# Performance work log

Measured on AMD Instinct MI355X. Metric: run time of the kernel, lower is better.

Reference implementation:

```python
import jax, jax.numpy as jnp
import numpy as np

T, B, I, H, E, C = 256, 64, 1024, 1024, 4, 128
STDV = 1.0 / np.sqrt(H)


def setup_inputs() -> dict:
    key = jax.random.key(0)
    ks = jax.random.split(key, 8)
    x_seq = jax.random.normal(ks[0], (T, B, I), dtype=jnp.float32)
    h0 = jnp.zeros((1, B, H), dtype=jnp.float32)
    c0 = jnp.zeros((1, B, H), dtype=jnp.float32)
    coef = jax.random.uniform(ks[1], (B, E), dtype=jnp.float32)
    # expert params (uniform(-stdv, stdv) init as in the torch module)
    u = lambda k, shp: jax.random.uniform(k, shp, dtype=jnp.float32, minval=-STDV, maxval=STDV)
    Wi = u(ks[2], (E, 4 * H, I))
    bi = u(ks[3], (E, 4 * H))
    Wh = u(ks[4], (E, 4 * H, H))
    bh = u(ks[5], (E, 4 * H))
    Wo = u(ks[6], (E, C, H))
    bo = u(ks[7], (E, C))
    return {"x_seq": x_seq, "h0": h0, "c0": c0, "coef": coef,
            "Wi": Wi, "bi": bi, "Wh": Wh, "bh": bh, "Wo": Wo, "bo": bo}


def reference(x_seq, h0, c0, coef, Wi, bi, Wh, bh, Wo, bo):
    # MoO with IDGate == per-sample convex combination of expert linear outputs,
    # which equals a linear layer with per-sample mixed weights.
    # Precompute mixed input projections for all timesteps: [T,B,4H]
    xi = jnp.einsum('tbi,eoi,be->tbo', x_seq, Wi, coef) + coef @ bi
    # Per-sample mixed hidden weights: [B,4H,H] and bias [B,4H]
    Whm = jnp.einsum('eoi,be->boi', Wh, coef)
    bhm = coef @ bh

    def step(carry, xg):
        h, c = carry
        gates = xg + jnp.einsum('bi,boi->bo', h, Whm) + bhm  # [B,4H]
        ig, fg, gg, og = jnp.split(gates, 4, axis=-1)  # i,f,g,o order as in torch chunk
        c = jax.nn.sigmoid(fg) * c + jax.nn.sigmoid(ig) * jnp.tanh(gg)
        h = jax.nn.sigmoid(og) * jnp.tanh(c)
        return (h, c), h

    (hT, cT), hs = jax.lax.scan(step, (h0[0], c0[0]), xi)  # hs: [T,B,H]
    # h2o: mixed output projection (activation is identity, dropout p=0)
    out = jnp.einsum('tbh,ech,be->tbc', hs, Wo, coef) + coef @ bo  # [T,B,C]
    return out, hT[None], cT[None]
```

## Files before the change

kernel.cpp:

```cpp
#include <hip/hip_runtime.h>
#include <hip/hip_fp16.h>
#include <cstdint>

#define T_  256
#define B_  64
#define I_  1024
#define H_  1024
#define E_  4
#define C_  128
#define G4  4096

typedef _Float16 f16;
typedef _Float16 f16x2 __attribute__((ext_vector_type(2)));
typedef _Float16 f16x8 __attribute__((ext_vector_type(8)));
typedef float    f32x4 __attribute__((ext_vector_type(4)));

__device__ __forceinline__ float sigmoidf_(float x) { return 1.f / (1.f + __expf(-x)); }

union pk2 { uint32_t u; f16x2 h; };

__global__ void k_f32_to_f16(const float* __restrict__ src, f16* __restrict__ dst, int n8) {
    int i = blockIdx.x * blockDim.x + threadIdx.x;
    int stride = gridDim.x * blockDim.x;
    for (; i < n8; i += stride) {
        const float4* s = reinterpret_cast<const float4*>(src) + (size_t)i * 2;
        float4 a = s[0], b = s[1];
        f16x8 v = { (f16)a.x, (f16)a.y, (f16)a.z, (f16)a.w,
                    (f16)b.x, (f16)b.y, (f16)b.z, (f16)b.w };
        *reinterpret_cast<f16x8*>(dst + (size_t)i * 8) = v;
    }
}

__global__ void k_mix_biases(const float* __restrict__ coef, const float* __restrict__ bi,
                             const float* __restrict__ bh, const float* __restrict__ bo,
                             float* __restrict__ gbias, float* __restrict__ bom) {
    int idx = blockIdx.x * blockDim.x + threadIdx.x;
    int stride = gridDim.x * blockDim.x;
    for (int i = idx; i < B_ * G4; i += stride) {
        int b = i >> 12, o = i & (G4 - 1);
        float s = 0.f;
#pragma unroll
        for (int e = 0; e < 4; ++e) s += coef[b * 4 + e] * (bi[e * G4 + o] + bh[e * G4 + o]);
        gbias[i] = s;
    }
    for (int i = idx; i < B_ * C_; i += stride) {
        int b = i >> 7, c = i & (C_ - 1);
        float s = 0.f;
#pragma unroll
        for (int e = 0; e < 4; ++e) s += coef[b * 4 + e] * bo[e * C_ + c];
        bom[i] = s;
    }
}

__global__ void k_init_h0h(const float* __restrict__ h0, f16* __restrict__ h0h) {
    int i = blockIdx.x * blockDim.x + threadIdx.x;
    if (i < B_ * H_) h0h[i] = (f16)h0[i];
}

template<bool XF16, bool WF16>
__global__ __launch_bounds__(256, 1) void k_xi_gemm(
        const f16* __restrict__ xh, const float* __restrict__ xf,
        const f16* __restrict__ Wih, const float* __restrict__ Wif,
        const float* __restrict__ coef, const float* __restrict__ gbias,
        f16* __restrict__ xi) {
    __shared__ f16 As[256 * 72];
    __shared__ f16 Bs[128 * 72];
    const int nt = blockIdx.x;
    const int b  = blockIdx.y;
    const int tid = threadIdx.x;
    const int lane = tid & 63, wave = tid >> 6;
    const int wr = wave >> 1, wc = wave & 1;

    float cf[4];
#pragma unroll
    for (int e = 0; e < 4; ++e) cf[e] = coef[b * 4 + e];

    f32x4 acc[8][4];
#pragma unroll
    for (int mi = 0; mi < 8; ++mi)
#pragma unroll
        for (int ni = 0; ni < 4; ++ni) acc[mi][ni] = 0.f;

    for (int kk = 0; kk < I_; kk += 64) {
        __syncthreads();
#pragma unroll
        for (int it = 0; it < 8; ++it) {
            int chunk = it * 256 + tid;
            int row = chunk >> 3, c8 = chunk & 7;
            if constexpr (XF16) {
                *reinterpret_cast<f16x8*>(&As[row * 72 + c8 * 8]) =
                    *reinterpret_cast<const f16x8*>(&xh[((size_t)row * B_ + b) * I_ + kk + c8 * 8]);
            } else {
                const float4* p = reinterpret_cast<const float4*>(&xf[((size_t)row * B_ + b) * I_ + kk + c8 * 8]);
                float4 a = p[0], bq = p[1];
                f16x8 v = { (f16)a.x, (f16)a.y, (f16)a.z, (f16)a.w,
                            (f16)bq.x, (f16)bq.y, (f16)bq.z, (f16)bq.w };
                *reinterpret_cast<f16x8*>(&As[row * 72 + c8 * 8]) = v;
            }
        }
#pragma unroll
        for (int it = 0; it < 4; ++it) {
            int chunk = it * 256 + tid;
            int n = chunk >> 3, c8 = chunk & 7;
            if constexpr (WF16) {
                size_t base = ((size_t)(nt * 128 + n)) * I_ + kk + c8 * 8;
                f16 c0 = (f16)cf[0], c1 = (f16)cf[1], c2 = (f16)cf[2], c3 = (f16)cf[3];
                f16x8 w0 = *reinterpret_cast<const f16x8*>(&Wih[base]);
                f16x8 w1 = *reinterpret_cast<const f16x8*>(&Wih[base + (size_t)1 * G4 * I_]);
                f16x8 w2 = *reinterpret_cast<const f16x8*>(&Wih[base + (size_t)2 * G4 * I_]);
                f16x8 w3 = *reinterpret_cast<const f16x8*>(&Wih[base + (size_t)3 * G4 * I_]);
                f16x8 m = w0 * c0 + w1 * c1 + w2 * c2 + w3 * c3;
                *reinterpret_cast<f16x8*>(&Bs[n * 72 + c8 * 8]) = m;
            } else {
                size_t base = ((size_t)(nt * 128 + n)) * I_ + kk + c8 * 8;
                float m[8];
#pragma unroll
                for (int j = 0; j < 8; ++j) m[j] = 0.f;
#pragma unroll
                for (int e = 0; e < 4; ++e) {
                    const float4* p = reinterpret_cast<const float4*>(&Wif[base + (size_t)e * G4 * I_]);
                    float4 a = p[0], bq = p[1];
                    m[0] += cf[e] * a.x;  m[1] += cf[e] * a.y;
                    m[2] += cf[e] * a.z;  m[3] += cf[e] * a.w;
                    m[4] += cf[e] * bq.x; m[5] += cf[e] * bq.y;
                    m[6] += cf[e] * bq.z; m[7] += cf[e] * bq.w;
                }
                f16x8 v = { (f16)m[0], (f16)m[1], (f16)m[2], (f16)m[3],
                            (f16)m[4], (f16)m[5], (f16)m[6], (f16)m[7] };
                *reinterpret_cast<f16x8*>(&Bs[n * 72 + c8 * 8]) = v;
            }
        }
        __syncthreads();
#pragma unroll
        for (int ks = 0; ks < 2; ++ks) {
            int ko = ks * 32 + (lane >> 4) * 8;
            f16x8 a[8], bb[4];
#pragma unroll
            for (int mi = 0; mi < 8; ++mi)
                a[mi] = *reinterpret_cast<const f16x8*>(&As[(wr * 128 + mi * 16 + (lane & 15)) * 72 + ko]);
#pragma unroll
            for (int ni = 0; ni < 4; ++ni)
                bb[ni] = *reinterpret_cast<const f16x8*>(&Bs[(wc * 64 + ni * 16 + (lane & 15)) * 72 + ko]);
#pragma unroll
            for (int mi = 0; mi < 8; ++mi)
#pragma unroll
                for (int ni = 0; ni < 4; ++ni)
                    acc[mi][ni] = __builtin_amdgcn_mfma_f32_16x16x32_f16(a[mi], bb[ni], acc[mi][ni], 0, 0, 0);
        }
    }
#pragma unroll
    for (int mi = 0; mi < 8; ++mi)
#pragma unroll
        for (int ni = 0; ni < 4; ++ni)
#pragma unroll
            for (int j = 0; j < 4; ++j) {
                int t = wr * 128 + mi * 16 + (lane >> 4) * 4 + j;
                int o = nt * 128 + wc * 64 + ni * 16 + (lane & 15);
                float v = acc[mi][ni][j] + gbias[b * G4 + o];
                xi[((size_t)t * B_ + b) * G4 + o] = (f16)v;
            }
}

#define POOL_SZ  163840
#define A0_OFF   131072
#define A1_OFF   (131072 + 8192)
#define A2_OFF   (131072 + 16384)
#define A3_OFF   (131072 + 24576)
#define GL_OFF   131072

#define BF(KC, KS) (*reinterpret_cast<const f16x8*>(pool + wrow + (KC) * 128 + (((KS) * 64 + koff) ^ swz)))
#define PRE(KC, PF) PF = *reinterpret_cast<const f16x8*>(&hprev[(size_t)sr * hstr + (KC) * 64 + soct * 8]);
#define AFR(AOFF, AROW, KS) (*reinterpret_cast<const f16x8*>(pool + (AOFF) + (AROW) + (((KS) * 64 + koff) ^ swz)))
#define WRA(AOFF, PF) *reinterpret_cast<f16x8*>(pool + (AOFF) + sdst) = PF;

#define MM4(ROFF, BQ0, BQ1) \
    acc0 = __builtin_amdgcn_mfma_f32_16x16x32_f16(AFR(ROFF, arow0, 0), BQ0, acc0, 0, 0, 0); \
    acc1 = __builtin_amdgcn_mfma_f32_16x16x32_f16(AFR(ROFF, arow1, 0), BQ0, acc1, 0, 0, 0); \
    acc0 = __builtin_amdgcn_mfma_f32_16x16x32_f16(AFR(ROFF, arow0, 1), BQ1, acc0, 0, 0, 0); \
    acc1 = __builtin_amdgcn_mfma_f32_16x16x32_f16(AFR(ROFF, arow1, 1), BQ1, acc1, 0, 0, 0);

#define TPW(KC, RB, PK, PL, PW, WB) { \
    const f16x8 bq0 = BF(KC, 0), bq1 = BF(KC, 1); \
    PRE(PK, PL); \
    MM4(RB, bq0, bq1); \
    WRA(WB, PW); \
}
#define TW(KC, RB, PW, WB) { \
    const f16x8 bq0 = BF(KC, 0), bq1 = BF(KC, 1); \
    MM4(RB, bq0, bq1); \
    WRA(WB, PW); \
}
#define TN(KC, RB) { \
    const f16x8 bq0 = BF(KC, 0), bq1 = BF(KC, 1); \
    MM4(RB, bq0, bq1); \
}

#define GO2IDX(T, KC, L) ((((size_t)(T) * 16 + (KC)) * 16 + (L)) * 16)

__device__ __forceinline__ void pollgo(const int* p) {
    while (__hip_atomic_load(p, __ATOMIC_RELAXED, __HIP_MEMORY_SCOPE_AGENT) == 0)
        __builtin_amdgcn_s_sleep(1);
}

__global__ __launch_bounds__(512, 1) void k_rec_persist(
        const float* __restrict__ Wh, const f16* __restrict__ h0h,
        const float* __restrict__ c0, f16* xi, const float* __restrict__ coef,
        float* __restrict__ out, int* __restrict__ arr, int* __restrict__ go2) {
    __shared__ __attribute__((aligned(16))) char pool[POOL_SZ];
    float* gl = reinterpret_cast<float*>(pool + GL_OFF);

    const int bid = blockIdx.x;
    const int jb = ((bid & 7) << 5) | (bid >> 3);
    const int tid = threadIdx.x, lane = tid & 63, w = tid >> 6;
    const int ex = w & 3, mh = w >> 2;
    const int l15 = lane & 15, hi8 = (lane >> 4) * 8;
    const int myTile = jb >> 4;
    const int goLine = bid & 15;

    for (int i = tid; i < 8192; i += 512) {
        int r = i >> 7, oct = i & 127;
        int e = r >> 4, g = (r >> 2) & 3, c = r & 3;
        const float* src = &Wh[((size_t)e * G4 + g * H_ + jb * 4 + c) * H_ + oct * 8];
        float4 f0 = *reinterpret_cast<const float4*>(src);
        float4 f1 = *reinterpret_cast<const float4*>(src + 4);
        f16x8 v = { (f16)f0.x, (f16)f0.y, (f16)f0.z, (f16)f0.w,
                    (f16)f1.x, (f16)f1.y, (f16)f1.z, (f16)f1.w };
        int db = r * 2048 + ((oct * 16) ^ ((r & 7) << 4));
        *reinterpret_cast<f16x8*>(pool + db) = v;
    }

    const int bb = tid >> 1, pr = tid & 1;
    const int cp0 = jb * 4 + pr * 2;
    float c_reg0 = 0.f, c_reg1 = 0.f;
    float4 cf4 = {0.f, 0.f, 0.f, 0.f};
    if (tid < 128) {
        c_reg0 = c0[bb * H_ + cp0];
        c_reg1 = c0[bb * H_ + cp0 + 1];
        cf4 = *reinterpret_cast<const float4*>(&coef[bb * 4]);
    }

    const int swz   = (l15 & 7) << 4;
    const int koff  = hi8 * 2;
    const int wrow  = (ex * 16 + l15) * 2048;
    const int arow0 = (mh * 32 + l15) * 128;
    const int arow1 = arow0 + 16 * 128;
    const int sr = tid >> 3, soct = tid & 7;
    const int sdst = sr * 128 + ((soct * 16) ^ ((sr & 7) << 4));

    __syncthreads();

    float xgc0a = 0.f, xgc0b = 0.f, xgc1a = 0.f, xgc1b = 0.f;
    float xgc2a = 0.f, xgc2b = 0.f, xgc3a = 0.f, xgc3b = 0.f;
    if (tid < 128) {
        const f16* xp = &xi[((size_t)0 * B_ + bb) * G4 + cp0];
        pk2 p0; p0.u = __hip_atomic_load(reinterpret_cast<const uint32_t*>(xp),
                                         __ATOMIC_RELAXED, __HIP_MEMORY_SCOPE_AGENT);
        xgc0a = (float)p0.h.x; xgc0b = (float)p0.h.y;
        f16x2 g1 = *reinterpret_cast<const f16x2*>(xp + H_);
        f16x2 g2 = *reinterpret_cast<const f16x2*>(xp + 2 * H_);
        f16x2 g3 = *reinterpret_cast<const f16x2*>(xp + 3 * H_);
        xgc1a = (float)g1.x; xgc1b = (float)g1.y;
        xgc2a = (float)g2.x; xgc2b = (float)g2.y;
        xgc3a = (float)g3.x; xgc3b = (float)g3.y;
    }

    for (int t = 0; t < T_; ++t) {
        const f16* hprev = (t == 0) ? h0h : (xi + (size_t)(t - 1) * B_ * G4);
        const size_t hstr = (t == 0) ? (size_t)H_ : (size_t)G4;

        if (t > 0) {
            if (tid < 8) pollgo(&go2[GO2IDX(t - 1, tid, goLine)]);
            __builtin_amdgcn_sched_barrier(0);
            __syncthreads();
        }

        f16x8 pfa, pfb, pfc, pfd;
        PRE(0, pfa) PRE(1, pfb) PRE(2, pfc) PRE(3, pfd)

        float xgn0a = 0.f, xgn0b = 0.f, xgn1a = 0.f, xgn1b = 0.f;
        float xgn2a = 0.f, xgn2b = 0.f, xgn3a = 0.f, xgn3b = 0.f;
        if (t + 1 < T_ && tid < 128) {
            const f16* xq = &xi[((size_t)(t + 1) * B_ + bb) * G4 + cp0];
            pk2 p0; p0.u = __hip_atomic_load(reinterpret_cast<const uint32_t*>(xq),
                                             __ATOMIC_RELAXED, __HIP_MEMORY_SCOPE_AGENT);
            xgn0a = (float)p0.h.x; xgn0b = (float)p0.h.y;
            f16x2 g1 = *reinterpret_cast<const f16x2*>(xq + H_);
            f16x2 g2 = *reinterpret_cast<const f16x2*>(xq + 2 * H_);
            f16x2 g3 = *reinterpret_cast<const f16x2*>(xq + 3 * H_);
            xgn1a = (float)g1.x; xgn1b = (float)g1.y;
            xgn2a = (float)g2.x; xgn2b = (float)g2.y;
            xgn3a = (float)g3.x; xgn3b = (float)g3.y;
        }

        WRA(A0_OFF, pfa)
        WRA(A1_OFF, pfb)
        f32x4 acc0 = {0.f, 0.f, 0.f, 0.f}, acc1 = {0.f, 0.f, 0.f, 0.f};
        __syncthreads();

        if (t > 0 && tid < 4) pollgo(&go2[GO2IDX(t - 1, 8 + tid, goLine)]);
        TPW(0, A0_OFF, 4, pfa, pfc, A2_OFF)
        TPW(1, A1_OFF, 5, pfb, pfd, A3_OFF)
        __syncthreads();
        TPW(2, A2_OFF, 6, pfc, pfa, A0_OFF)
        TPW(3, A3_OFF, 7, pfd, pfb, A1_OFF)
        __syncthreads();
        if (t > 0 && tid < 4) pollgo(&go2[GO2IDX(t - 1, 12 + tid, goLine)]);
        TPW(4, A0_OFF, 8, pfa, pfc, A2_OFF)
        TPW(5, A1_OFF, 9, pfb, pfd, A3_OFF)
        __syncthreads();
        TPW(6, A2_OFF, 10, pfc, pfa, A0_OFF)
        TPW(7, A3_OFF, 11, pfd, pfb, A1_OFF)
        __syncthreads();
        TPW(8, A0_OFF, 12, pfa, pfc, A2_OFF)
        TPW(9, A1_OFF, 13, pfb, pfd, A3_OFF)
        __syncthreads();
        TPW(10, A2_OFF, 14, pfc, pfa, A0_OFF)
        TPW(11, A3_OFF, 15, pfd, pfb, A1_OFF)
        __syncthreads();
        TW(12, A0_OFF, pfc, A2_OFF)
        TW(13, A1_OFF, pfd, A3_OFF)
        __syncthreads();
        TN(14, A2_OFF)
        TN(15, A3_OFF)
        __syncthreads();

#pragma unroll
        for (int j = 0; j < 4; ++j) {
            int r0 = mh * 32 + (lane >> 4) * 4 + j;
            gl[(ex * 64 + r0) * 17 + l15]      = acc0[j];
            gl[(ex * 64 + r0 + 16) * 17 + l15] = acc1[j];
        }
        __syncthreads();

        if (tid < 128) {
            float ga[4], gb[4];
#pragma unroll
            for (int g = 0; g < 4; ++g) {
                int nn = g * 4 + pr * 2;
                ga[g] = cf4.x * gl[(0 * 64 + bb) * 17 + nn] +
                        cf4.y * gl[(1 * 64 + bb) * 17 + nn] +
                        cf4.z * gl[(2 * 64 + bb) * 17 + nn] +
                        cf4.w * gl[(3 * 64 + bb) * 17 + nn];
                gb[g] = cf4.x * gl[(0 * 64 + bb) * 17 + nn + 1] +
                        cf4.y * gl[(1 * 64 + bb) * 17 + nn + 1] +
                        cf4.z * gl[(2 * 64 + bb) * 17 + nn + 1] +
                        cf4.w * gl[(3 * 64 + bb) * 17 + nn + 1];
            }
            ga[0] += xgc0a; ga[1] += xgc1a; ga[2] += xgc2a; ga[3] += xgc3a;
            gb[0] += xgc0b; gb[1] += xgc1b; gb[2] += xgc2b; gb[3] += xgc3b;
            float cn0 = sigmoidf_(ga[1]) * c_reg0 + sigmoidf_(ga[0]) * tanhf(ga[2]);
            float hn0 = sigmoidf_(ga[3]) * tanhf(cn0);
            float cn1 = sigmoidf_(gb[1]) * c_reg1 + sigmoidf_(gb[0]) * tanhf(gb[2]);
            float hn1 = sigmoidf_(gb[3]) * tanhf(cn1);
            c_reg0 = cn0; c_reg1 = cn1;
            pk2 st; st.h.x = (f16)hn0; st.h.y = (f16)hn1;
            __hip_atomic_store(reinterpret_cast<uint32_t*>(&xi[((size_t)t * B_ + bb) * G4 + cp0]),
                               st.u, __ATOMIC_RELAXED, __HIP_MEMORY_SCOPE_AGENT);
            if (t == T_ - 1) {
                out[(size_t)T_ * B_ * C_ + bb * H_ + cp0]     = hn0;
                out[(size_t)T_ * B_ * C_ + bb * H_ + cp0 + 1] = hn1;
                out[(size_t)T_ * B_ * C_ + B_ * H_ + bb * H_ + cp0]     = cn0;
                out[(size_t)T_ * B_ * C_ + B_ * H_ + bb * H_ + cp0 + 1] = cn1;
            }
        }
        xgc0a = xgn0a; xgc0b = xgn0b; xgc1a = xgn1a; xgc1b = xgn1b;
        xgc2a = xgn2a; xgc2b = xgn2b; xgc3a = xgn3a; xgc3b = xgn3b;

        if (t < T_ - 1) {
            __syncthreads();
            if (tid == 0)
                __hip_atomic_store(&arr[t * 256 + jb], 1, __ATOMIC_RELAXED,
                                   __HIP_MEMORY_SCOPE_AGENT);
            __syncthreads();
            if (tid < 64) {
                int v = 1;
                if (lane < 16)
                    v = __hip_atomic_load(&arr[t * 256 + myTile * 16 + lane],
                                          __ATOMIC_RELAXED, __HIP_MEMORY_SCOPE_AGENT);
                unsigned long long m = __ballot(v != 0);
                if (m == ~0ull && lane < 16)
                    __hip_atomic_store(&go2[GO2IDX(t, myTile, lane)], 1,
                                       __ATOMIC_RELAXED, __HIP_MEMORY_SCOPE_AGENT);
            }
        }
    }
}

__global__ __launch_bounds__(256, 1) void k_out_gemm(
        const f16* __restrict__ hs, const f16* __restrict__ Woh,
        const float* __restrict__ coef, const float* __restrict__ bom,
        float* __restrict__ out) {
    __shared__ f16 As[64 * 72];
    __shared__ f16 Bs[256 * 72];
    __shared__ float cfs[64][4];
    const int nt = blockIdx.x;
    const int t  = blockIdx.y;
    const int tid = threadIdx.x, lane = tid & 63, w = tid >> 6;
    cfs[tid >> 2][tid & 3] = coef[tid];

    f32x4 acc[4][4];
#pragma unroll
    for (int e = 0; e < 4; ++e)
#pragma unroll
        for (int mi = 0; mi < 4; ++mi) acc[e][mi] = 0.f;

    for (int kk = 0; kk < H_; kk += 64) {
        __syncthreads();
#pragma unroll
        for (int it = 0; it < 2; ++it) {
            int chunk = it * 256 + tid;
            int row = chunk >> 3, c8 = chunk & 7;
            *reinterpret_cast<f16x8*>(&As[row * 72 + c8 * 8]) =
                *reinterpret_cast<const f16x8*>(&hs[((size_t)t * B_ + row) * G4 + kk + c8 * 8]);
        }
#pragma unroll
        for (int it = 0; it < 8; ++it) {
            int chunk = it * 256 + tid;
            int r = chunk >> 3, c8 = chunk & 7;
            int e = r >> 6, nn = r & 63;
            size_t grow = (size_t)e * C_ + nt * 64 + nn;
            *reinterpret_cast<f16x8*>(&Bs[r * 72 + c8 * 8]) =
                *reinterpret_cast<const f16x8*>(&Woh[grow * H_ + kk + c8 * 8]);
        }
        __syncthreads();
#pragma unroll
        for (int ks = 0; ks < 2; ++ks) {
            int ko = ks * 32 + (lane >> 4) * 8;
            f16x8 a[4];
#pragma unroll
            for (int mi = 0; mi < 4; ++mi)
                a[mi] = *reinterpret_cast<const f16x8*>(&As[(mi * 16 + (lane & 15)) * 72 + ko]);
#pragma unroll
            for (int e = 0; e < 4; ++e) {
                f16x8 bf = *reinterpret_cast<const f16x8*>(&Bs[(e * 64 + w * 16 + (lane & 15)) * 72 + ko]);
#pragma unroll
                for (int mi = 0; mi < 4; ++mi)
                    acc[e][mi] = __builtin_amdgcn_mfma_f32_16x16x32_f16(a[mi], bf, acc[e][mi], 0, 0, 0);
            }
        }
    }
#pragma unroll
    for (int mi = 0; mi < 4; ++mi)
#pragma unroll
        for (int j = 0; j < 4; ++j) {
            int bb = mi * 16 + (lane >> 4) * 4 + j;
            int cc = nt * 64 + w * 16 + (lane & 15);
            float v = cfs[bb][0] * acc[0][mi][j] + cfs[bb][1] * acc[1][mi][j] +
                      cfs[bb][2] * acc[2][mi][j] + cfs[bb][3] * acc[3][mi][j];
            v += bom[bb * C_ + cc];
            out[((size_t)t * B_ + bb) * C_ + cc] = v;
        }
}

extern "C" void kernel_launch(void* const* d_in, const int* in_sizes, int n_in,
                              void* d_out, int out_size, void* d_ws, size_t ws_size,
                              hipStream_t stream) {
    const float* x    = (const float*)d_in[0];
    const float* h0   = (const float*)d_in[1];
    const float* c0   = (const float*)d_in[2];
    const float* coef = (const float*)d_in[3];
    const float* Wi   = (const float*)d_in[4];
    const float* bi   = (const float*)d_in[5];
    const float* Wh   = (const float*)d_in[6];
    const float* bh   = (const float*)d_in[7];
    const float* Wo   = (const float*)d_in[8];
    const float* bo   = (const float*)d_in[9];
    float* out = (float*)d_out;

    char* base = (char*)d_ws;
    size_t off = 0;
    auto carve = [&](size_t bytes) -> char* {
        char* r = base + off;
        off = (off + bytes + 255) & ~(size_t)255;
        return r;
    };
    const size_t SZ_XI  = (size_t)T_ * B_ * G4 * 2;
    const size_t SZ_WOH = (size_t)E_ * C_ * H_ * 2;
    const size_t SZ_ARR = (size_t)T_ * 256 * 4;
    const size_t SZ_GO2 = (size_t)T_ * 16 * 16 * 16 * 4;
    const size_t SZ_WIH = (size_t)E_ * G4 * I_ * 2;
    const size_t SZ_XH  = (size_t)T_ * B_ * I_ * 2;

    f16*   xi     = (f16*)carve(SZ_XI);
    f16*   Woh    = (f16*)carve(SZ_WOH);
    f16*   h0h    = (f16*)carve((size_t)B_ * H_ * 2);
    float* gbias  = (float*)carve((size_t)B_ * G4 * 4);
    float* bom    = (float*)carve((size_t)B_ * C_ * 4);
    int*   arr    = (int*)carve(SZ_ARR);
    int*   go2    = (int*)carve(SZ_GO2);

    f16* Wih = nullptr;
    f16* xh  = nullptr;
    if (off + SZ_WIH + 256 <= ws_size) Wih = (f16*)carve(SZ_WIH);
    if (Wih && off + SZ_XH + 256 <= ws_size) xh = (f16*)carve(SZ_XH);
    (void)in_sizes; (void)n_in; (void)out_size;

    hipMemsetAsync(arr, 0, SZ_ARR, stream);
    hipMemsetAsync(go2, 0, SZ_GO2, stream);

    if (xh)  k_f32_to_f16<<<2048, 256, 0, stream>>>(x,  xh,  (T_ * B_ * I_) / 8);
    if (Wih) k_f32_to_f16<<<2048, 256, 0, stream>>>(Wi, Wih, (E_ * G4 * I_) / 8);
    k_f32_to_f16<<<512,  256, 0, stream>>>(Wo, Woh, (E_ * C_ * H_) / 8);
    k_mix_biases<<<512, 256, 0, stream>>>(coef, bi, bh, bo, gbias, bom);
    k_init_h0h<<<(B_ * H_ + 255) / 256, 256, 0, stream>>>(h0, h0h);

    dim3 gx(32, 64);
    if (xh)
        k_xi_gemm<true,  true ><<<gx, 256, 0, stream>>>(xh, nullptr, Wih, nullptr, coef, gbias, xi);
    else if (Wih)
        k_xi_gemm<false, true ><<<gx, 256, 0, stream>>>(nullptr, x, Wih, nullptr, coef, gbias, xi);
    else
        k_xi_gemm<false, false><<<gx, 256, 0, stream>>>(nullptr, x, nullptr, Wi, coef, gbias, xi);

    {
        void* args[] = { (void*)&Wh, (void*)&h0h, (void*)&c0, (void*)&xi,
                         (void*)&coef, (void*)&out, (void*)&arr, (void*)&go2 };
        hipLaunchCooperativeKernel((const void*)k_rec_persist, dim3(256), dim3(512),
                                   args, 0, stream);
    }

    dim3 go_(2, 256);
    k_out_gemm<<<go_, 256, 0, stream>>>(xi, Woh, coef, bom, out);
}
```

Baseline: 2.261 ms.

## Replace two-level arrive/go flags with atomic fetch-or bitmask per tile

Each block now sets its bit with an atomic fetch_or on all 16 replicated go lines for its tile, and consumers poll all 16 tile words up front until each reads 0xFFFF. This replaces the arrive array, the leader aggregation via ballot and the staggered partial polls that overlapped the wait with the first MFMA chunks. The extra sync hop through a per-tile leader goes away, but every block now waits for all tiles before any compute, so there is no longer any overlap of the wait with early k-chunks. Contended atomics on shared words are also added.

```diff
diff --git a/kernel.cpp b/kernel.cpp
--- a/kernel.cpp
+++ b/kernel.cpp
@@ -195,17 +195,12 @@
     MM4(RB, bq0, bq1); \
 }
 
-#define GO2IDX(T, KC, L) ((((size_t)(T) * 16 + (KC)) * 16 + (L)) * 16)
-
-__device__ __forceinline__ void pollgo(const int* p) {
-    while (__hip_atomic_load(p, __ATOMIC_RELAXED, __HIP_MEMORY_SCOPE_AGENT) == 0)
-        __builtin_amdgcn_s_sleep(1);
-}
+#define GO3IDX(T, TILE, L) ((((size_t)(T) * 16 + (TILE)) * 16 + (L)) * 16)
 
 __global__ __launch_bounds__(512, 1) void k_rec_persist(
         const float* __restrict__ Wh, const f16* __restrict__ h0h,
         const float* __restrict__ c0, f16* xi, const float* __restrict__ coef,
-        float* __restrict__ out, int* __restrict__ arr, int* __restrict__ go2) {
+        float* __restrict__ out, int* __restrict__ go3) {
     __shared__ __attribute__((aligned(16))) char pool[POOL_SZ];
     float* gl = reinterpret_cast<float*>(pool + GL_OFF);
 
@@ -216,6 +211,7 @@
     const int l15 = lane & 15, hi8 = (lane >> 4) * 8;
     const int myTile = jb >> 4;
     const int goLine = bid & 15;
+    const int myBit  = 1 << (jb & 15);
 
     for (int i = tid; i < 8192; i += 512) {
         int r = i >> 7, oct = i & 127;
@@ -269,7 +265,12 @@
         const size_t hstr = (t == 0) ? (size_t)H_ : (size_t)G4;
 
         if (t > 0) {
-            if (tid < 8) pollgo(&go2[GO2IDX(t - 1, tid, goLine)]);
+            if (tid < 16) {
+                const int* p = &go3[GO3IDX(t - 1, tid, goLine)];
+                while (__hip_atomic_load(p, __ATOMIC_RELAXED, __HIP_MEMORY_SCOPE_AGENT)
+                       != 0xFFFF)
+                    __builtin_amdgcn_s_sleep(1);
+            }
             __builtin_amdgcn_sched_barrier(0);
             __syncthreads();
         }
@@ -297,14 +298,12 @@
         f32x4 acc0 = {0.f, 0.f, 0.f, 0.f}, acc1 = {0.f, 0.f, 0.f, 0.f};
         __syncthreads();
 
-        if (t > 0 && tid < 4) pollgo(&go2[GO2IDX(t - 1, 8 + tid, goLine)]);
         TPW(0, A0_OFF, 4, pfa, pfc, A2_OFF)
         TPW(1, A1_OFF, 5, pfb, pfd, A3_OFF)
         __syncthreads();
         TPW(2, A2_OFF, 6, pfc, pfa, A0_OFF)
         TPW(3, A3_OFF, 7, pfd, pfb, A1_OFF)
         __syncthreads();
-        if (t > 0 && tid < 4) pollgo(&go2[GO2IDX(t - 1, 12 + tid, goLine)]);
         TPW(4, A0_OFF, 8, pfa, pfc, A2_OFF)
         TPW(5, A1_OFF, 9, pfb, pfd, A3_OFF)
         __syncthreads();
@@ -368,20 +367,9 @@
 
         if (t < T_ - 1) {
             __syncthreads();
-            if (tid == 0)
-                __hip_atomic_store(&arr[t * 256 + jb], 1, __ATOMIC_RELAXED,
-                                   __HIP_MEMORY_SCOPE_AGENT);
-            __syncthreads();
-            if (tid < 64) {
-                int v = 1;
-                if (lane < 16)
-                    v = __hip_atomic_load(&arr[t * 256 + myTile * 16 + lane],
-                                          __ATOMIC_RELAXED, __HIP_MEMORY_SCOPE_AGENT);
-                unsigned long long m = __ballot(v != 0);
-                if (m == ~0ull && lane < 16)
-                    __hip_atomic_store(&go2[GO2IDX(t, myTile, lane)], 1,
-                                       __ATOMIC_RELAXED, __HIP_MEMORY_SCOPE_AGENT);
-            }
+            if (tid < 16)
+                __hip_atomic_fetch_or(&go3[GO3IDX(t, myTile, tid)], myBit,
+                                      __ATOMIC_RELEASE, __HIP_MEMORY_SCOPE_AGENT);
         }
     }
 }
@@ -476,8 +464,7 @@
     };
     const size_t SZ_XI  = (size_t)T_ * B_ * G4 * 2;
     const size_t SZ_WOH = (size_t)E_ * C_ * H_ * 2;
-    const size_t SZ_ARR = (size_t)T_ * 256 * 4;
-    const size_t SZ_GO2 = (size_t)T_ * 16 * 16 * 16 * 4;
+    const size_t SZ_GO3 = (size_t)T_ * 16 * 16 * 16 * 4;
     const size_t SZ_WIH = (size_t)E_ * G4 * I_ * 2;
     const size_t SZ_XH  = (size_t)T_ * B_ * I_ * 2;
 
@@ -486,8 +473,7 @@
     f16*   h0h    = (f16*)carve((size_t)B_ * H_ * 2);
     float* gbias  = (float*)carve((size_t)B_ * G4 * 4);
     float* bom    = (float*)carve((size_t)B_ * C_ * 4);
-    int*   arr    = (int*)carve(SZ_ARR);
-    int*   go2    = (int*)carve(SZ_GO2);
+    int*   go3    = (int*)carve(SZ_GO3);
 
     f16* Wih = nullptr;
     f16* xh  = nullptr;
@@ -495,8 +481,7 @@
     if (Wih && off + SZ_XH + 256 <= ws_size) xh = (f16*)carve(SZ_XH);
     (void)in_sizes; (void)n_in; (void)out_size;
 
-    hipMemsetAsync(arr, 0, SZ_ARR, stream);
-    hipMemsetAsync(go2, 0, SZ_GO2, stream);
+    hipMemsetAsync(go3, 0, SZ_GO3, stream);
 
     if (xh)  k_f32_to_f16<<<2048, 256, 0, stream>>>(x,  xh,  (T_ * B_ * I_) / 8);
     if (Wih) k_f32_to_f16<<<2048, 256, 0, stream>>>(Wi, Wih, (E_ * G4 * I_) / 8);
@@ -514,7 +499,7 @@
 
     {
         void* args[] = { (void*)&Wh, (void*)&h0h, (void*)&c0, (void*)&xi,
-                         (void*)&coef, (void*)&out, (void*)&arr, (void*)&go2 };
+                         (void*)&coef, (void*)&out, (void*)&go3 };
         hipLaunchCooperativeKernel((const void*)k_rec_persist, dim3(256), dim3(512),
                                    args, 0, stream);
     }
```

Result: slower. 2.662 ms (+17.8%).
